# Performance work log

Hardware: AMD Instinct MI355X
Metric: run time of the kernel (lower is better)

## Reference

```python
import jax, jax.numpy as jnp
import numpy as np

B, T, R = 64, 256, 256          # batch, timepoints, n_rois (T==R required by bmm path)
H, NH, DH, FF, LAT, L = 256, 8, 32, 512, 64, 2
EPS = 1e-5


def layernorm(x, g, b):
    m = x.mean(-1, keepdims=True)
    v = ((x - m) ** 2).mean(-1, keepdims=True)
    return (x - m) / jnp.sqrt(v + EPS) * g + b


def leaky_relu(x):
    return jnp.where(x >= 0, x, 0.1 * x)


def setup_inputs() -> dict:
    key = jax.random.key(0)
    ks = iter(jax.random.split(key, 64))
    def nrm(shape, s=0.02):
        return jax.random.normal(next(ks), shape, jnp.float32) * s
    return {
        "x": jax.random.normal(next(ks), (B, T, R), jnp.float32),
        "node_view": jax.random.normal(next(ks), (B, R, R), jnp.float32) * 0.1,
        "edge_view": jax.random.normal(next(ks), (B, R, R), jnp.float32) * 0.1,
        "fp_w": nrm((H, R)), "fp_b": jnp.zeros((H,)),
        "fp_g": jnp.ones((H,)), "fp_beta": jnp.zeros((H,)),
        "qkv_w": nrm((L, 3 * H, H)), "qkv_b": jnp.zeros((L, 3 * H)),
        "attn_out_w": nrm((L, H, H)), "attn_out_b": jnp.zeros((L, H)),
        "ln1_g": jnp.ones((L, H)), "ln1_b": jnp.zeros((L, H)),
        "ff1_w": nrm((L, FF, H)), "ff1_b": jnp.zeros((L, FF)),
        "ff2_w": nrm((L, H, FF)), "ff2_b": jnp.zeros((L, H)),
        "ln2_g": jnp.ones((L, H)), "ln2_b": jnp.zeros((L, H)),
        "out_w": nrm((R, H)), "out_b": jnp.zeros((R,)),
        "mu_w1": nrm((H // 2, H)), "mu_b1": jnp.zeros((H // 2,)),
        "mu_g": jnp.ones((H // 2,)), "mu_beta": jnp.zeros((H // 2,)),
        "mu_w2": nrm((LAT, H // 2)), "mu_b2": jnp.zeros((LAT,)),
        "lv_w1": nrm((H // 2, H)), "lv_b1": jnp.zeros((H // 2,)),
        "lv_g": jnp.ones((H // 2,)), "lv_beta": jnp.zeros((H // 2,)),
        "lv_w2": nrm((LAT, H // 2)), "lv_b2": jnp.zeros((LAT,)),
    }


def reference(x, node_view, edge_view, fp_w, fp_b, fp_g, fp_beta,
              qkv_w, qkv_b, attn_out_w, attn_out_b, ln1_g, ln1_b,
              ff1_w, ff1_b, ff2_w, ff2_b, ln2_g, ln2_b,
              out_w, out_b, mu_w1, mu_b1, mu_g, mu_beta, mu_w2, mu_b2,
              lv_w1, lv_b1, lv_g, lv_beta, lv_w2, lv_b2):
    # graph-view message passing: bmm(x^T, view), averaged, transposed back
    xr = jnp.swapaxes(x, 1, 2)                           # [B,R,T]
    msg = 0.5 * (jnp.einsum('brt,btq->brq', xr, node_view)
                 + jnp.einsum('brt,btq->brq', xr, edge_view))
    h = jnp.swapaxes(msg, 1, 2)                          # [B,T,R]
    # feature_proj: Linear -> LayerNorm -> LeakyReLU(0.1) -> Dropout(eval)
    h = leaky_relu(layernorm(h @ fp_w.T + fp_b, fp_g, fp_beta))  # [B,T,H]
    # TransformerEncoder (post-norm, relu FFN, dropout=identity)
    scale = 1.0 / jnp.sqrt(jnp.float32(DH))
    for i in range(L):
        qkv = h @ qkv_w[i].T + qkv_b[i]                  # [B,T,3H]
        q, k, v = jnp.split(qkv, 3, axis=-1)
        q = q.reshape(B, T, NH, DH).transpose(0, 2, 1, 3)
        k = k.reshape(B, T, NH, DH).transpose(0, 2, 1, 3)
        v = v.reshape(B, T, NH, DH).transpose(0, 2, 1, 3)
        attn = jax.nn.softmax(jnp.einsum('bhqd,bhkd->bhqk', q, k) * scale, axis=-1)
        o = jnp.einsum('bhqk,bhkd->bhqd', attn, v).transpose(0, 2, 1, 3).reshape(B, T, H)
        o = o @ attn_out_w[i].T + attn_out_b[i]
        h = layernorm(h + o, ln1_g[i], ln1_b[i])
        f = jax.nn.relu(h @ ff1_w[i].T + ff1_b[i]) @ ff2_w[i].T + ff2_b[i]
        h = layernorm(h + f, ln2_g[i], ln2_b[i])
    # fresh linear (treated as fixed params) then batched Pearson correlation
    y = h @ out_w.T + out_b                              # [B,T,R]
    data = jnp.swapaxes(y, 1, 2)                         # [B,R,T]
    c = data - data.mean(-1, keepdims=True)
    std = jnp.sqrt((c ** 2).sum(-1, keepdims=True) / (T - 1))   # unbiased, like torch.std
    cn = c / (std + 1e-8)
    corr = jnp.einsum('brt,bst->brs', cn, cn) / (T - 1)
    corr = jnp.nan_to_num(jnp.clip(corr, -1.0, 1.0), nan=0.0)   # [B,R,R]
    # heads
    pooled = h.mean(axis=1)                              # [B,H]
    mu = leaky_relu(layernorm(pooled @ mu_w1.T + mu_b1, mu_g, mu_beta)) @ mu_w2.T + mu_b2
    logvar = leaky_relu(layernorm(pooled @ lv_w1.T + lv_b1, lv_g, lv_beta)) @ lv_w2.T + lv_b2
    return mu, logvar, corr
```

## Files before the change

### kernel.cpp

```cpp
#include <hip/hip_runtime.h>
#include <hip/hip_bf16.h>
#include <math.h>

#define BB 64
#define NLAYER 2

typedef __attribute__((ext_vector_type(8))) short bfrag;
typedef __attribute__((ext_vector_type(4))) float f4_t;

__device__ __forceinline__ float dot4(float4 a, float4 b, float acc) {
    acc = fmaf(a.x, b.x, acc);
    acc = fmaf(a.y, b.y, acc);
    acc = fmaf(a.z, b.z, acc);
    acc = fmaf(a.w, b.w, acc);
    return acc;
}

__device__ __forceinline__ ushort f2bf(float f) {
    uint32_t u = __float_as_uint(f);
    uint32_t r = (u + 0x7FFFu + ((u >> 16) & 1u)) >> 16;
    return (ushort)r;
}
__device__ __forceinline__ float bf2f(ushort u) {
    return __uint_as_float(((uint32_t)u) << 16);
}

__global__ __launch_bounds__(256) void k_cvt(
    const float* __restrict__ fp_w, const float* __restrict__ qkv_w,
    const float* __restrict__ aow, const float* __restrict__ f1w,
    const float* __restrict__ f2w, const float* __restrict__ outw,
    ushort* __restrict__ dst) {
    const int g = blockIdx.x;
    const size_t idx = (size_t)g * 2048 + threadIdx.x * 8;
    const float* src;
    size_t base;
    if (g < 32)       { src = fp_w;  base = 0; }
    else if (g < 224) { src = qkv_w; base = 65536; }
    else if (g < 288) { src = aow;   base = 458752; }
    else if (g < 416) { src = f1w;   base = 589824; }
    else if (g < 544) { src = f2w;   base = 851968; }
    else              { src = outw;  base = 1114112; }
    const float4* s4 = reinterpret_cast<const float4*>(src + (idx - base));
    float4 a = s4[0], b = s4[1];
    bfrag o;
    o[0] = (short)f2bf(a.x); o[1] = (short)f2bf(a.y);
    o[2] = (short)f2bf(a.z); o[3] = (short)f2bf(a.w);
    o[4] = (short)f2bf(b.x); o[5] = (short)f2bf(b.y);
    o[6] = (short)f2bf(b.z); o[7] = (short)f2bf(b.w);
    *reinterpret_cast<bfrag*>(dst + idx) = o;
}

template <int EPI, bool WF32, bool WBF>
__global__ __launch_bounds__(256) void k_mm(
    const ushort* __restrict__ A, const ushort* __restrict__ B,
    const float* __restrict__ bias, float* __restrict__ C,
    ushort* __restrict__ Cb, int K, int N,
    size_t aStr, size_t bStr, size_t cStr) {
    __shared__ __align__(16) ushort As[64 * 72];
    __shared__ __align__(16) ushort Bs[128 * 72];
    const int tid = threadIdx.x;
    const int m0 = blockIdx.x * 64, n0 = blockIdx.y * 128;
    const size_t z = blockIdx.z;
    const int w = tid >> 6, lane = tid & 63;
    const int wm = w >> 1, wn = w & 1;
    const int fr = lane & 15, fq = lane >> 4;

    const int arow = tid >> 2, akc = (tid & 3) * 16;
    const ushort* aS = A + z * aStr + (size_t)(m0 + arow) * K + akc;
    ushort* aD = &As[arow * 72 + akc];
    const int brow = tid >> 1, bkc = (tid & 1) * 32;
    const ushort* bS = B + z * bStr + (size_t)(n0 + brow) * K + bkc;
    ushort* bD = &Bs[brow * 72 + bkc];

    f4_t acc[2][4];
#pragma unroll
    for (int i = 0; i < 2; ++i)
#pragma unroll
        for (int j = 0; j < 4; ++j) acc[i][j] = (f4_t)0.f;

    bfrag ra0, ra1, rb0, rb1, rb2, rb3;
    {
        const bfrag* ap = reinterpret_cast<const bfrag*>(aS);
        ra0 = ap[0]; ra1 = ap[1];
        const bfrag* bp = reinterpret_cast<const bfrag*>(bS);
        rb0 = bp[0]; rb1 = bp[1]; rb2 = bp[2]; rb3 = bp[3];
    }

    for (int k0 = 0; k0 < K; k0 += 64) {
        reinterpret_cast<bfrag*>(aD)[0] = ra0;
        reinterpret_cast<bfrag*>(aD)[1] = ra1;
        reinterpret_cast<bfrag*>(bD)[0] = rb0;
        reinterpret_cast<bfrag*>(bD)[1] = rb1;
        reinterpret_cast<bfrag*>(bD)[2] = rb2;
        reinterpret_cast<bfrag*>(bD)[3] = rb3;
        __syncthreads();
        if (k0 + 64 < K) {
            const bfrag* ap = reinterpret_cast<const bfrag*>(aS + k0 + 64);
            ra0 = ap[0]; ra1 = ap[1];
            const bfrag* bp = reinterpret_cast<const bfrag*>(bS + k0 + 64);
            rb0 = bp[0]; rb1 = bp[1]; rb2 = bp[2]; rb3 = bp[3];
        }
#pragma unroll
        for (int ks = 0; ks < 2; ++ks) {
            const int kb = ks * 32 + fq * 8;
            bfrag af[2], bf[4];
#pragma unroll
            for (int fm = 0; fm < 2; ++fm)
                af[fm] = *reinterpret_cast<const bfrag*>(
                    &As[(wm * 32 + fm * 16 + fr) * 72 + kb]);
#pragma unroll
            for (int fn = 0; fn < 4; ++fn)
                bf[fn] = *reinterpret_cast<const bfrag*>(
                    &Bs[(wn * 64 + fn * 16 + fr) * 72 + kb]);
#pragma unroll
            for (int fm = 0; fm < 2; ++fm)
#pragma unroll
                for (int fn = 0; fn < 4; ++fn)
                    acc[fm][fn] = __builtin_amdgcn_mfma_f32_16x16x32_bf16(
                        bf[fn], af[fm], acc[fm][fn], 0, 0, 0);
        }
        __syncthreads();
    }

#pragma unroll
    for (int fn = 0; fn < 4; ++fn) {
        const int col0 = n0 + wn * 64 + fn * 16 + fq * 4;
        float4 bv = make_float4(0.f, 0.f, 0.f, 0.f);
        if (bias != nullptr)
            bv = *reinterpret_cast<const float4*>(&bias[col0]);
#pragma unroll
        for (int fm = 0; fm < 2; ++fm) {
            const int row = m0 + wm * 32 + fm * 16 + fr;
            float v0 = acc[fm][fn][0] + bv.x;
            float v1 = acc[fm][fn][1] + bv.y;
            float v2 = acc[fm][fn][2] + bv.z;
            float v3 = acc[fm][fn][3] + bv.w;
            if (EPI == 2) {
                v0 = fmaxf(v0, 0.f); v1 = fmaxf(v1, 0.f);
                v2 = fmaxf(v2, 0.f); v3 = fmaxf(v3, 0.f);
            }
            const size_t o = cStr * z + (size_t)row * N + col0;
            if (WF32) {
                float4 fv = {v0, v1, v2, v3};
                *reinterpret_cast<float4*>(&C[o]) = fv;
            }
            if (WBF) {
                ushort4 uv;
                uv.x = f2bf(v0); uv.y = f2bf(v1);
                uv.z = f2bf(v2); uv.w = f2bf(v3);
                *reinterpret_cast<ushort4*>(&Cb[o]) = uv;
            }
        }
    }
}

__global__ __launch_bounds__(256) void k_mmqkv(
    const ushort* __restrict__ A, const ushort* __restrict__ B,
    const float* __restrict__ bias, ushort* __restrict__ qb,
    ushort* __restrict__ kbuf, ushort* __restrict__ vtb) {
    __shared__ __align__(16) ushort As[64 * 72];
    __shared__ __align__(16) ushort Bs[128 * 72];
    const int tid = threadIdx.x;
    const int m0 = blockIdx.x * 64, n0 = blockIdx.y * 128;
    const int w = tid >> 6, lane = tid & 63;
    const int wm = w >> 1, wn = w & 1;
    const int fr = lane & 15, fq = lane >> 4;
    const int K = 256;

    const int arow = tid >> 2, akc = (tid & 3) * 16;
    const ushort* aS = A + (size_t)(m0 + arow) * K + akc;
    ushort* aD = &As[arow * 72 + akc];
    const int brow = tid >> 1, bkc = (tid & 1) * 32;
    const ushort* bS = B + (size_t)(n0 + brow) * K + bkc;
    ushort* bD = &Bs[brow * 72 + bkc];

    f4_t acc[2][4];
#pragma unroll
    for (int i = 0; i < 2; ++i)
#pragma unroll
        for (int j = 0; j < 4; ++j) acc[i][j] = (f4_t)0.f;

    bfrag ra0, ra1, rb0, rb1, rb2, rb3;
    {
        const bfrag* ap = reinterpret_cast<const bfrag*>(aS);
        ra0 = ap[0]; ra1 = ap[1];
        const bfrag* bp = reinterpret_cast<const bfrag*>(bS);
        rb0 = bp[0]; rb1 = bp[1]; rb2 = bp[2]; rb3 = bp[3];
    }

    for (int k0 = 0; k0 < K; k0 += 64) {
        reinterpret_cast<bfrag*>(aD)[0] = ra0;
        reinterpret_cast<bfrag*>(aD)[1] = ra1;
        reinterpret_cast<bfrag*>(bD)[0] = rb0;
        reinterpret_cast<bfrag*>(bD)[1] = rb1;
        reinterpret_cast<bfrag*>(bD)[2] = rb2;
        reinterpret_cast<bfrag*>(bD)[3] = rb3;
        __syncthreads();
        if (k0 + 64 < K) {
            const bfrag* ap = reinterpret_cast<const bfrag*>(aS + k0 + 64);
            ra0 = ap[0]; ra1 = ap[1];
            const bfrag* bp = reinterpret_cast<const bfrag*>(bS + k0 + 64);
            rb0 = bp[0]; rb1 = bp[1]; rb2 = bp[2]; rb3 = bp[3];
        }
#pragma unroll
        for (int ks = 0; ks < 2; ++ks) {
            const int kb = ks * 32 + fq * 8;
            bfrag af[2], bf[4];
#pragma unroll
            for (int fm = 0; fm < 2; ++fm)
                af[fm] = *reinterpret_cast<const bfrag*>(
                    &As[(wm * 32 + fm * 16 + fr) * 72 + kb]);
#pragma unroll
            for (int fn = 0; fn < 4; ++fn)
                bf[fn] = *reinterpret_cast<const bfrag*>(
                    &Bs[(wn * 64 + fn * 16 + fr) * 72 + kb]);
#pragma unroll
            for (int fm = 0; fm < 2; ++fm)
#pragma unroll
                for (int fn = 0; fn < 4; ++fn)
                    acc[fm][fn] = __builtin_amdgcn_mfma_f32_16x16x32_bf16(
                        bf[fn], af[fm], acc[fm][fn], 0, 0, 0);
        }
        __syncthreads();
    }

    const int sec = n0 >> 8;
#pragma unroll
    for (int fn = 0; fn < 4; ++fn) {
        const int col0 = n0 + wn * 64 + fn * 16 + fq * 4;
        const int hd = (col0 >> 5) & 7, dq = col0 & 31;
        const float4 bv = *reinterpret_cast<const float4*>(&bias[col0]);
#pragma unroll
        for (int fm = 0; fm < 2; ++fm) {
            const int row = m0 + wm * 32 + fm * 16 + fr;
            const int b = row >> 8, t = row & 255;
            const size_t bh = (size_t)b * 8 + hd;
            float v0 = acc[fm][fn][0] + bv.x;
            float v1 = acc[fm][fn][1] + bv.y;
            float v2 = acc[fm][fn][2] + bv.z;
            float v3 = acc[fm][fn][3] + bv.w;
            if (sec < 2) {
                ushort4 uv;
                uv.x = f2bf(v0); uv.y = f2bf(v1);
                uv.z = f2bf(v2); uv.w = f2bf(v3);
                ushort* dst = (sec == 0 ? qb : kbuf) + (bh * 256 + t) * 32 + dq;
                *reinterpret_cast<ushort4*>(dst) = uv;
            } else {
                ushort* dst = vtb + (bh * 32 + dq) * 256 + t;
                dst[0] = f2bf(v0);
                dst[256] = f2bf(v1);
                dst[512] = f2bf(v2);
                dst[768] = f2bf(v3);
            }
        }
    }
}

template <int ACT, bool RES>
__global__ __launch_bounds__(256) void k_mmln(
    const ushort* __restrict__ A, const ushort* __restrict__ W,
    const float* __restrict__ bias, const ushort* __restrict__ res,
    const float* __restrict__ g, const float* __restrict__ bt,
    ushort* __restrict__ outb, int K) {
    __shared__ __align__(16) ushort As[32 * 72];
    __shared__ __align__(16) ushort Bs[256 * 72];
    __shared__ float redS[32][4];
    __shared__ float redQ[32][4];
    const int tid = threadIdx.x;
    const int m0 = blockIdx.x * 32;
    const int w = tid >> 6, lane = tid & 63;
    const int fr = lane & 15, fq = lane >> 4;

    const int arow = tid >> 3, akc = (tid & 7) * 8;
    const ushort* aS = A + (size_t)(m0 + arow) * K + akc;
    ushort* aD = &As[arow * 72 + akc];
    const int brow = tid >> 1, bkc = (tid & 1) * 32;
    const ushort* bS0 = W + (size_t)brow * K + bkc;
    const ushort* bS1 = W + (size_t)(brow + 128) * K + bkc;
    ushort* bD0 = &Bs[brow * 72 + bkc];
    ushort* bD1 = &Bs[(brow + 128) * 72 + bkc];

    f4_t acc[2][4];
#pragma unroll
    for (int i = 0; i < 2; ++i)
#pragma unroll
        for (int j = 0; j < 4; ++j) acc[i][j] = (f4_t)0.f;

    bfrag ra, rb0, rb1, rb2, rb3, rc0, rc1, rc2, rc3;
    {
        ra = *reinterpret_cast<const bfrag*>(aS);
        const bfrag* bp0 = reinterpret_cast<const bfrag*>(bS0);
        rb0 = bp0[0]; rb1 = bp0[1]; rb2 = bp0[2]; rb3 = bp0[3];
        const bfrag* bp1 = reinterpret_cast<const bfrag*>(bS1);
        rc0 = bp1[0]; rc1 = bp1[1]; rc2 = bp1[2]; rc3 = bp1[3];
    }

    for (int k0 = 0; k0 < K; k0 += 64) {
        *reinterpret_cast<bfrag*>(aD) = ra;
        reinterpret_cast<bfrag*>(bD0)[0] = rb0;
        reinterpret_cast<bfrag*>(bD0)[1] = rb1;
        reinterpret_cast<bfrag*>(bD0)[2] = rb2;
        reinterpret_cast<bfrag*>(bD0)[3] = rb3;
        reinterpret_cast<bfrag*>(bD1)[0] = rc0;
        reinterpret_cast<bfrag*>(bD1)[1] = rc1;
        reinterpret_cast<bfrag*>(bD1)[2] = rc2;
        reinterpret_cast<bfrag*>(bD1)[3] = rc3;
        __syncthreads();
        if (k0 + 64 < K) {
            ra = *reinterpret_cast<const bfrag*>(aS + k0 + 64);
            const bfrag* bp0 = reinterpret_cast<const bfrag*>(bS0 + k0 + 64);
            rb0 = bp0[0]; rb1 = bp0[1]; rb2 = bp0[2]; rb3 = bp0[3];
            const bfrag* bp1 = reinterpret_cast<const bfrag*>(bS1 + k0 + 64);
            rc0 = bp1[0]; rc1 = bp1[1]; rc2 = bp1[2]; rc3 = bp1[3];
        }
#pragma unroll
        for (int ks = 0; ks < 2; ++ks) {
            const int kb = ks * 32 + fq * 8;
            bfrag af[2], bf[4];
#pragma unroll
            for (int fm = 0; fm < 2; ++fm)
                af[fm] = *reinterpret_cast<const bfrag*>(
                    &As[(fm * 16 + fr) * 72 + kb]);
#pragma unroll
            for (int fn = 0; fn < 4; ++fn)
                bf[fn] = *reinterpret_cast<const bfrag*>(
                    &Bs[(w * 64 + fn * 16 + fr) * 72 + kb]);
#pragma unroll
            for (int fm = 0; fm < 2; ++fm)
#pragma unroll
                for (int fn = 0; fn < 4; ++fn)
                    acc[fm][fn] = __builtin_amdgcn_mfma_f32_16x16x32_bf16(
                        bf[fn], af[fm], acc[fm][fn], 0, 0, 0);
        }
        __syncthreads();
    }

#pragma unroll
    for (int fn = 0; fn < 4; ++fn) {
        const int col0 = w * 64 + fn * 16 + fq * 4;
        const float4 bv = *reinterpret_cast<const float4*>(&bias[col0]);
#pragma unroll
        for (int fm = 0; fm < 2; ++fm) {
            const int row = fm * 16 + fr;
            float r0 = 0.f, r1 = 0.f, r2 = 0.f, r3 = 0.f;
            if (RES) {
                ushort4 r4 = *reinterpret_cast<const ushort4*>(
                    &res[(size_t)(m0 + row) * 256 + col0]);
                r0 = bf2f(r4.x); r1 = bf2f(r4.y);
                r2 = bf2f(r4.z); r3 = bf2f(r4.w);
            }
            acc[fm][fn][0] += bv.x + r0;
            acc[fm][fn][1] += bv.y + r1;
            acc[fm][fn][2] += bv.z + r2;
            acc[fm][fn][3] += bv.w + r3;
        }
    }
#pragma unroll
    for (int fm = 0; fm < 2; ++fm) {
        float s = 0.f, q = 0.f;
#pragma unroll
        for (int fn = 0; fn < 4; ++fn)
#pragma unroll
            for (int j = 0; j < 4; ++j) {
                const float v = acc[fm][fn][j];
                s += v;
                q += v * v;
            }
        s += __shfl_xor(s, 16); q += __shfl_xor(q, 16);
        s += __shfl_xor(s, 32); q += __shfl_xor(q, 32);
        if (fq == 0) {
            redS[fm * 16 + fr][w] = s;
            redQ[fm * 16 + fr][w] = q;
        }
    }
    __syncthreads();
#pragma unroll
    for (int fm = 0; fm < 2; ++fm) {
        const int row = fm * 16 + fr;
        const float S = redS[row][0] + redS[row][1] + redS[row][2] + redS[row][3];
        const float Q = redQ[row][0] + redQ[row][1] + redQ[row][2] + redQ[row][3];
        const float mean = S * (1.f / 256.f);
        const float var = Q * (1.f / 256.f) - mean * mean;
        const float rstd = rsqrtf(fmaxf(var, 0.f) + 1e-5f);
        const size_t rowoff = (size_t)(m0 + row) * 256;
#pragma unroll
        for (int fn = 0; fn < 4; ++fn) {
            const int col0 = w * 64 + fn * 16 + fq * 4;
            const float4 g4 = *reinterpret_cast<const float4*>(&g[col0]);
            const float4 b4 = *reinterpret_cast<const float4*>(&bt[col0]);
            float v0 = (acc[fm][fn][0] - mean) * rstd * g4.x + b4.x;
            float v1 = (acc[fm][fn][1] - mean) * rstd * g4.y + b4.y;
            float v2 = (acc[fm][fn][2] - mean) * rstd * g4.z + b4.z;
            float v3 = (acc[fm][fn][3] - mean) * rstd * g4.w + b4.w;
            if (ACT == 1) {
                v0 = v0 >= 0.f ? v0 : 0.1f * v0;
                v1 = v1 >= 0.f ? v1 : 0.1f * v1;
                v2 = v2 >= 0.f ? v2 : 0.1f * v2;
                v3 = v3 >= 0.f ? v3 : 0.1f * v3;
            }
            ushort4 uv;
            uv.x = f2bf(v0); uv.y = f2bf(v1);
            uv.z = f2bf(v2); uv.w = f2bf(v3);
            *reinterpret_cast<ushort4*>(&outb[rowoff + col0]) = uv;
        }
    }
}

__global__ __launch_bounds__(256) void k_attn3(
    const ushort* __restrict__ qb, const ushort* __restrict__ kbuf,
    const ushort* __restrict__ vtb, ushort* __restrict__ o) {
    __shared__ __align__(16) ushort Ps[4][64][40];
    const int hd = blockIdx.x, b = blockIdx.y;
    const size_t bh = (size_t)b * 8 + hd;
    const int tid = threadIdx.x;
    const int w = tid >> 6, lane = tid & 63;
    const int fr = lane & 15, fq = lane >> 4;

    const ushort* qB = qb + bh * 8192;
    const ushort* kB = kbuf + bh * 8192;
    const ushort* vB = vtb + bh * 8192;

    const int q0 = w * 64;
    bfrag qf[4];
#pragma unroll
    for (int fm = 0; fm < 4; ++fm)
        qf[fm] = *reinterpret_cast<const bfrag*>(
            qB + (size_t)(q0 + fm * 16 + fr) * 32 + fq * 8);

    f4_t oacc[4][2];
    float rs[4][4];
#pragma unroll
    for (int fm = 0; fm < 4; ++fm) {
        oacc[fm][0] = (f4_t)0.f;
        oacc[fm][1] = (f4_t)0.f;
#pragma unroll
        for (int j = 0; j < 4; ++j) rs[fm][j] = 0.f;
    }
    const f4_t zero4 = (f4_t)0.f;
    const float qsl = 0.17677669529663687f * 1.4426950408889634f;

    for (int kt = 0; kt < 8; ++kt) {
        bfrag kf0 = *reinterpret_cast<const bfrag*>(
            kB + (size_t)(kt * 32 + fr) * 32 + fq * 8);
        bfrag kf1 = *reinterpret_cast<const bfrag*>(
            kB + (size_t)(kt * 32 + 16 + fr) * 32 + fq * 8);
        f4_t s0[4], s1[4];
#pragma unroll
        for (int fm = 0; fm < 4; ++fm) {
            s0[fm] = __builtin_amdgcn_mfma_f32_16x16x32_bf16(qf[fm], kf0, zero4, 0, 0, 0);
            s1[fm] = __builtin_amdgcn_mfma_f32_16x16x32_bf16(qf[fm], kf1, zero4, 0, 0, 0);
        }
#pragma unroll
        for (int fm = 0; fm < 4; ++fm) {
#pragma unroll
            for (int j = 0; j < 4; ++j) {
                const int row = fm * 16 + fq * 4 + j;
                ushort u0 = f2bf(exp2f(s0[fm][j] * qsl));
                ushort u1 = f2bf(exp2f(s1[fm][j] * qsl));
                Ps[w][row][fr] = u0;
                Ps[w][row][16 + fr] = u1;
                rs[fm][j] += bf2f(u0) + bf2f(u1);
            }
        }
        bfrag vf0 = *reinterpret_cast<const bfrag*>(
            vB + (size_t)fr * 256 + kt * 32 + fq * 8);
        bfrag vf1 = *reinterpret_cast<const bfrag*>(
            vB + (size_t)(16 + fr) * 256 + kt * 32 + fq * 8);
        bfrag pf[4];
#pragma unroll
        for (int fm = 0; fm < 4; ++fm)
            pf[fm] = *reinterpret_cast<const bfrag*>(&Ps[w][fm * 16 + fr][fq * 8]);
#pragma unroll
        for (int fm = 0; fm < 4; ++fm) {
            oacc[fm][0] = __builtin_amdgcn_mfma_f32_16x16x32_bf16(pf[fm], vf0, oacc[fm][0], 0, 0, 0);
            oacc[fm][1] = __builtin_amdgcn_mfma_f32_16x16x32_bf16(pf[fm], vf1, oacc[fm][1], 0, 0, 0);
        }
    }

#pragma unroll
    for (int fm = 0; fm < 4; ++fm)
#pragma unroll
        for (int j = 0; j < 4; ++j) {
            float r = rs[fm][j];
            r += __shfl_xor(r, 1);
            r += __shfl_xor(r, 2);
            r += __shfl_xor(r, 4);
            r += __shfl_xor(r, 8);
            rs[fm][j] = 1.f / r;
        }
    ushort* ob = o + (size_t)b * 65536 + hd * 32;
#pragma unroll
    for (int fm = 0; fm < 4; ++fm) {
        const int qrow = q0 + fm * 16 + fq * 4;
#pragma unroll
        for (int j = 0; j < 4; ++j) {
            const float inv = rs[fm][j];
            ob[(size_t)(qrow + j) * 256 + fr] = f2bf(oacc[fm][0][j] * inv);
            ob[(size_t)(qrow + j) * 256 + 16 + fr] = f2bf(oacc[fm][1][j] * inv);
        }
    }
}

__global__ __launch_bounds__(256) void k_xpose_bmm(
    const float* __restrict__ x, const float* __restrict__ nv,
    const float* __restrict__ ev, ushort* __restrict__ At,
    ushort* __restrict__ Xt) {
    const int b = blockIdx.z;
    const int k0 = blockIdx.x * 64, i0 = blockIdx.y * 64;
    __shared__ float TA[64][65];
    __shared__ float TX[64][65];
    const size_t bb = (size_t)b * 65536;
    const int tid = threadIdx.x;
    const int lr = tid >> 4, lc = (tid & 15) * 4;
#pragma unroll
    for (int l = 0; l < 4; ++l) {
        const int row = lr + l * 16;
        const size_t gidx = bb + (size_t)(k0 + row) * 256 + i0 + lc;
        float4 n4 = *reinterpret_cast<const float4*>(nv + gidx);
        float4 e4 = *reinterpret_cast<const float4*>(ev + gidx);
        float4 x4 = *reinterpret_cast<const float4*>(x + gidx);
        TA[row][lc] = 0.5f * (n4.x + e4.x);
        TA[row][lc + 1] = 0.5f * (n4.y + e4.y);
        TA[row][lc + 2] = 0.5f * (n4.z + e4.z);
        TA[row][lc + 3] = 0.5f * (n4.w + e4.w);
        TX[row][lc] = x4.x;
        TX[row][lc + 1] = x4.y;
        TX[row][lc + 2] = x4.z;
        TX[row][lc + 3] = x4.w;
    }
    __syncthreads();
    const int i = tid & 63, kk = (tid >> 6) * 16;
    bfrag a0, a1, x0, x1;
#pragma unroll
    for (int e = 0; e < 8; ++e) {
        a0[e] = (short)f2bf(TA[kk + e][i]);
        a1[e] = (short)f2bf(TA[kk + 8 + e][i]);
        x0[e] = (short)f2bf(TX[kk + e][i]);
        x1[e] = (short)f2bf(TX[kk + 8 + e][i]);
    }
    const size_t o = bb + (size_t)(i0 + i) * 256 + k0 + kk;
    *reinterpret_cast<bfrag*>(At + o) = a0;
    *reinterpret_cast<bfrag*>(At + o + 8) = a1;
    *reinterpret_cast<bfrag*>(Xt + o) = x0;
    *reinterpret_cast<bfrag*>(Xt + o + 8) = x1;
}

__global__ __launch_bounds__(256) void k_rowstats(const ushort* __restrict__ yT,
                                                  float* __restrict__ stats) {
    const int b = blockIdx.y;
    const int r = blockIdx.x * 64 + (threadIdx.x >> 2);
    const int part = threadIdx.x & 3;
    const ushort* row = yT + (size_t)b * 65536 + (size_t)r * 256 + part * 64;
    float s = 0.f, q = 0.f;
#pragma unroll
    for (int i = 0; i < 8; ++i) {
        bfrag v = reinterpret_cast<const bfrag*>(row)[i];
#pragma unroll
        for (int e = 0; e < 8; ++e) {
            float f = bf2f((ushort)v[e]);
            s += f;
            q += f * f;
        }
    }
    s += __shfl_xor(s, 1); q += __shfl_xor(q, 1);
    s += __shfl_xor(s, 2); q += __shfl_xor(q, 2);
    if (part == 0) {
        const float mean = s * (1.f / 256.f);
        const float var = (q - s * mean) * (1.f / 255.f);
        const float stdv = sqrtf(fmaxf(var, 0.f));
        stats[b * 512 + r] = mean;
        stats[b * 512 + 256 + r] = 1.f / (stdv + 1e-8f);
    }
}

__global__ __launch_bounds__(256) void k_corr2(
    const ushort* __restrict__ A, const float* __restrict__ stats,
    float* __restrict__ C) {
    __shared__ __align__(16) ushort As[64 * 72];
    __shared__ __align__(16) ushort Bs[128 * 72];
    const int tid = threadIdx.x;
    const int m0 = blockIdx.x * 64, n0 = blockIdx.y * 128;
    const size_t z = blockIdx.z;
    const int w = tid >> 6, lane = tid & 63;
    const int wm = w >> 1, wn = w & 1;
    const int fr = lane & 15, fq = lane >> 4;
    const int K = 256;

    const int arow = tid >> 2, akc = (tid & 3) * 16;
    const ushort* aS = A + z * 65536 + (size_t)(m0 + arow) * K + akc;
    ushort* aD = &As[arow * 72 + akc];
    const int brow = tid >> 1, bkc = (tid & 1) * 32;
    const ushort* bS = A + z * 65536 + (size_t)(n0 + brow) * K + bkc;
    ushort* bD = &Bs[brow * 72 + bkc];

    f4_t acc[2][4];
#pragma unroll
    for (int i = 0; i < 2; ++i)
#pragma unroll
        for (int j = 0; j < 4; ++j) acc[i][j] = (f4_t)0.f;

    bfrag ra0, ra1, rb0, rb1, rb2, rb3;
    {
        const bfrag* ap = reinterpret_cast<const bfrag*>(aS);
        ra0 = ap[0]; ra1 = ap[1];
        const bfrag* bp = reinterpret_cast<const bfrag*>(bS);
        rb0 = bp[0]; rb1 = bp[1]; rb2 = bp[2]; rb3 = bp[3];
    }

    for (int k0 = 0; k0 < K; k0 += 64) {
        reinterpret_cast<bfrag*>(aD)[0] = ra0;
        reinterpret_cast<bfrag*>(aD)[1] = ra1;
        reinterpret_cast<bfrag*>(bD)[0] = rb0;
        reinterpret_cast<bfrag*>(bD)[1] = rb1;
        reinterpret_cast<bfrag*>(bD)[2] = rb2;
        reinterpret_cast<bfrag*>(bD)[3] = rb3;
        __syncthreads();
        if (k0 + 64 < K) {
            const bfrag* ap = reinterpret_cast<const bfrag*>(aS + k0 + 64);
            ra0 = ap[0]; ra1 = ap[1];
            const bfrag* bp = reinterpret_cast<const bfrag*>(bS + k0 + 64);
            rb0 = bp[0]; rb1 = bp[1]; rb2 = bp[2]; rb3 = bp[3];
        }
#pragma unroll
        for (int ks = 0; ks < 2; ++ks) {
            const int kb = ks * 32 + fq * 8;
            bfrag af[2], bf[4];
#pragma unroll
            for (int fm = 0; fm < 2; ++fm)
                af[fm] = *reinterpret_cast<const bfrag*>(
                    &As[(wm * 32 + fm * 16 + fr) * 72 + kb]);
#pragma unroll
            for (int fn = 0; fn < 4; ++fn)
                bf[fn] = *reinterpret_cast<const bfrag*>(
                    &Bs[(wn * 64 + fn * 16 + fr) * 72 + kb]);
#pragma unroll
            for (int fm = 0; fm < 2; ++fm)
#pragma unroll
                for (int fn = 0; fn < 4; ++fn)
                    acc[fm][fn] = __builtin_amdgcn_mfma_f32_16x16x32_bf16(
                        bf[fn], af[fm], acc[fm][fn], 0, 0, 0);
        }
        __syncthreads();
    }

    const float* st = stats + z * 512;
#pragma unroll
    for (int fn = 0; fn < 4; ++fn) {
        const int col0 = n0 + wn * 64 + fn * 16 + fq * 4;
        const float4 muj = *reinterpret_cast<const float4*>(&st[col0]);
        const float4 isj = *reinterpret_cast<const float4*>(&st[256 + col0]);
#pragma unroll
        for (int fm = 0; fm < 2; ++fm) {
            const int row = m0 + wm * 32 + fm * 16 + fr;
            const float mui = st[row];
            const float isi = st[256 + row] * (1.f / 255.f);
            float v0 = (acc[fm][fn][0] - 256.f * mui * muj.x) * isi * isj.x;
            float v1 = (acc[fm][fn][1] - 256.f * mui * muj.y) * isi * isj.y;
            float v2 = (acc[fm][fn][2] - 256.f * mui * muj.z) * isi * isj.z;
            float v3 = (acc[fm][fn][3] - 256.f * mui * muj.w) * isi * isj.w;
            if (v0 != v0) v0 = 0.f;
            if (v1 != v1) v1 = 0.f;
            if (v2 != v2) v2 = 0.f;
            if (v3 != v3) v3 = 0.f;
            v0 = fminf(1.f, fmaxf(-1.f, v0));
            v1 = fminf(1.f, fmaxf(-1.f, v1));
            v2 = fminf(1.f, fmaxf(-1.f, v2));
            v3 = fminf(1.f, fmaxf(-1.f, v3));
            float4 fv = {v0, v1, v2, v3};
            *reinterpret_cast<float4*>(
                &C[z * 65536 + (size_t)row * 256 + col0]) = fv;
        }
    }
}

__global__ __launch_bounds__(512) void k_poolhead(
    const ushort* __restrict__ h,
    const float* __restrict__ mw1, const float* __restrict__ mb1,
    const float* __restrict__ mg, const float* __restrict__ mbt,
    const float* __restrict__ mw2, const float* __restrict__ mb2,
    const float* __restrict__ lw1, const float* __restrict__ lb1,
    const float* __restrict__ lg, const float* __restrict__ lbt,
    const float* __restrict__ lw2, const float* __restrict__ lb2,
    float* __restrict__ outp) {
    const int b = blockIdx.x, tid = threadIdx.x;
    __shared__ float pp[2][256];
    __shared__ float pooled[256];
    __shared__ float rS[4], rQ[4];
    __shared__ float t1[2][128];

    {
        const int c = tid & 255, tc = tid >> 8;
        const ushort* hb = h + (size_t)b * 65536 + (size_t)tc * 128 * 256 + c;
        float s = 0.f;
        for (int t = 0; t < 128; ++t) s += bf2f(hb[(size_t)t * 256]);
        pp[tc][c] = s;
    }
    __syncthreads();
    if (tid < 256) pooled[tid] = (pp[0][tid] + pp[1][tid]) * (1.f / 256.f);
    __syncthreads();

    float a = 0.f;
    if (tid < 256) {
        const int hd = tid >> 7, u = tid & 127;
        const float* w1 = hd ? lw1 : mw1;
        const float* b1 = hd ? lb1 : mb1;
        a = b1[u];
        const float4* w1v = reinterpret_cast<const float4*>(w1 + (size_t)u * 256);
#pragma unroll 4
        for (int k4 = 0; k4 < 64; ++k4) {
            float4 wv = w1v[k4];
            float4 p = *reinterpret_cast<const float4*>(&pooled[k4 * 4]);
            a = dot4(p, wv, a);
        }
        float s = a, q = a * a;
#pragma unroll
        for (int m = 1; m < 64; m <<= 1) {
            s += __shfl_xor(s, m);
            q += __shfl_xor(q, m);
        }
        if ((tid & 63) == 0) { rS[tid >> 6] = s; rQ[tid >> 6] = q; }
    }
    __syncthreads();
    if (tid < 256) {
        const int hd = tid >> 7, u = tid & 127;
        const float* g = hd ? lg : mg;
        const float* bt = hd ? lbt : mbt;
        const float S = rS[hd * 2] + rS[hd * 2 + 1];
        const float Q = rQ[hd * 2] + rQ[hd * 2 + 1];
        const float mean = S * (1.f / 128.f);
        const float var = Q * (1.f / 128.f) - mean * mean;
        const float rstd = rsqrtf(fmaxf(var, 0.f) + 1e-5f);
        float v = (a - mean) * rstd * g[u] + bt[u];
        v = v >= 0.f ? v : 0.1f * v;
        t1[hd][u] = v;
    }
    __syncthreads();
    if (tid < 128) {
        const int hd = tid >> 6, ou = tid & 63;
        const float* w2 = hd ? lw2 : mw2;
        const float* b2 = hd ? lb2 : mb2;
        float o = b2[ou];
        const float* w2r = w2 + (size_t)ou * 128;
#pragma unroll 4
        for (int c = 0; c < 128; ++c) o = fmaf(t1[hd][c], w2r[c], o);
        outp[hd * 4096 + b * 64 + ou] = o;
    }
}

extern "C" void kernel_launch(void* const* d_in, const int* in_sizes, int n_in,
                              void* d_out, int out_size, void* d_ws, size_t ws_size,
                              hipStream_t stream) {
    const float* x = (const float*)d_in[0];
    const float* nv = (const float*)d_in[1];
    const float* ev = (const float*)d_in[2];
    const float* fp_w = (const float*)d_in[3];
    const float* fp_b = (const float*)d_in[4];
    const float* fp_g = (const float*)d_in[5];
    const float* fp_beta = (const float*)d_in[6];
    const float* qkv_w = (const float*)d_in[7];
    const float* qkv_b = (const float*)d_in[8];
    const float* aow = (const float*)d_in[9];
    const float* aob = (const float*)d_in[10];
    const float* ln1g = (const float*)d_in[11];
    const float* ln1b = (const float*)d_in[12];
    const float* f1w = (const float*)d_in[13];
    const float* f1b = (const float*)d_in[14];
    const float* f2w = (const float*)d_in[15];
    const float* f2b = (const float*)d_in[16];
    const float* ln2g = (const float*)d_in[17];
    const float* ln2b = (const float*)d_in[18];
    const float* outw = (const float*)d_in[19];
    const float* outb = (const float*)d_in[20];
    const float* muw1 = (const float*)d_in[21];
    const float* mub1 = (const float*)d_in[22];
    const float* mug = (const float*)d_in[23];
    const float* mubt = (const float*)d_in[24];
    const float* muw2 = (const float*)d_in[25];
    const float* mub2 = (const float*)d_in[26];
    const float* lvw1 = (const float*)d_in[27];
    const float* lvb1 = (const float*)d_in[28];
    const float* lvg = (const float*)d_in[29];
    const float* lvbt = (const float*)d_in[30];
    const float* lvw2 = (const float*)d_in[31];
    const float* lvb2 = (const float*)d_in[32];

    float* out = (float*)d_out;
    float* ws = (float*)d_ws;

    float* stats = ws;
    ushort* ub = (ushort*)(ws + 32768);
    ushort* wh_bf = ub;
    ushort* At = ub + 4194304;
    ushort* Xt = ub + 8388608;
    ushort* o_bf = ub + 16777216;
    ushort* h0_bf = o_bf;
    ushort* f1_bf = ub + 20971520;
    ushort* qb = ub + 29360128;
    ushort* kb = ub + 33554432;
    ushort* vtb = ub + 37748736;
    ushort* yT = ub + 41943040;
    ushort* wbf = ub + 46137344;

    k_cvt<<<576, 256, 0, stream>>>(fp_w, qkv_w, aow, f1w, f2w, outw, wbf);

    k_xpose_bmm<<<dim3(4, 4, BB), 256, 0, stream>>>(x, nv, ev, At, Xt);
    k_mm<0, false, true><<<dim3(4, 2, BB), 256, 0, stream>>>(
        At, Xt, nullptr, nullptr, h0_bf, 256, 256, 65536, 65536, 65536);

    k_mmln<1, false><<<512, 256, 0, stream>>>(
        h0_bf, wbf, fp_b, nullptr, fp_g, fp_beta, wh_bf, 256);

    for (int l = 0; l < NLAYER; ++l) {
        k_mmqkv<<<dim3(256, 6), 256, 0, stream>>>(
            wh_bf, wbf + 65536 + (size_t)l * 196608, qkv_b + l * 768,
            qb, kb, vtb);
        k_attn3<<<dim3(8, BB), 256, 0, stream>>>(qb, kb, vtb, o_bf);
        k_mmln<0, true><<<512, 256, 0, stream>>>(
            o_bf, wbf + 458752 + (size_t)l * 65536, aob + l * 256,
            wh_bf, ln1g + l * 256, ln1b + l * 256, wh_bf, 256);
        k_mm<2, false, true><<<dim3(256, 4, 1), 256, 0, stream>>>(
            wh_bf, wbf + 589824 + (size_t)l * 131072, f1b + l * 512,
            nullptr, f1_bf, 256, 512, 0, 0, 0);
        k_mmln<0, true><<<512, 256, 0, stream>>>(
            f1_bf, wbf + 851968 + (size_t)l * 131072, f2b + l * 256,
            wh_bf, ln2g + l * 256, ln2b + l * 256, wh_bf, 512);
    }

    k_mm<0, false, true><<<dim3(4, 2, BB), 256, 0, stream>>>(
        wbf + 1114112, wh_bf, nullptr, nullptr, yT, 256, 256, 0, 65536, 65536);

    k_rowstats<<<dim3(4, BB), 256, 0, stream>>>(yT, stats);
    k_corr2<<<dim3(4, 2, BB), 256, 0, stream>>>(yT, stats, out + 8192);

    k_poolhead<<<BB, 512, 0, stream>>>(
        wh_bf, muw1, mub1, mug, mubt, muw2, mub2,
        lvw1, lvb1, lvg, lvbt, lvw2, lvb2, out);
}
```

Baseline: 239.1 us.

## Use direct global-to-LDS loads and 128x128 tiles in GEMM kernels

Replaces the register-staged, padded-LDS GEMM loads with `__builtin_amdgcn_global_load_lds` direct copies into an unpadded 64-wide LDS layout. The output tile grows from 64x128 to 128x128, so each wave computes 4x4 MFMA fragments. This applies to the generic matmul, the QKV projection and the correlation kernel, with grids halved to match. It aims to cut VGPR staging and raise arithmetic intensity per block. In exchange it drops the register prefetch of the next K slice, halves the number of blocks, and the unpadded layout may cause LDS bank conflicts on fragment reads.

```diff
diff --git a/kernel.cpp b/kernel.cpp
--- a/kernel.cpp
+++ b/kernel.cpp
@@ -23,6 +23,12 @@
 }
 __device__ __forceinline__ float bf2f(ushort u) {
     return __uint_as_float(((uint32_t)u) << 16);
+}
+
+__device__ __forceinline__ void gll16(const ushort* g, ushort* l) {
+    __builtin_amdgcn_global_load_lds(
+        (const __attribute__((address_space(1))) void*)g,
+        (__attribute__((address_space(3))) void*)l, 16, 0, 0);
 }
 
 __global__ __launch_bounds__(256) void k_cvt(
@@ -50,75 +56,66 @@
     *reinterpret_cast<bfrag*>(dst + idx) = o;
 }
 
+#define MM97_STAGE(SRC, LDS, KSTRIDE)                                        \
+    {                                                                        \
+        _Pragma("unroll")                                                    \
+        for (int c = 0; c < 4; ++c) {                                        \
+            const int rr = (w << 5) + (c << 3) + (lane >> 3);                \
+            gll16(SRC + (size_t)rr * (KSTRIDE) + k0 + ((lane & 7) << 3),     \
+                  LDS + (((w << 5) + (c << 3)) << 6));                       \
+        }                                                                    \
+    }
+
+#define MM97_COMPUTE()                                                       \
+    _Pragma("unroll")                                                        \
+    for (int ks = 0; ks < 2; ++ks) {                                         \
+        const int kb = ks * 32 + fq * 8;                                     \
+        bfrag af[4], bfv[4];                                                 \
+        _Pragma("unroll")                                                    \
+        for (int fm = 0; fm < 4; ++fm)                                       \
+            af[fm] = *reinterpret_cast<const bfrag*>(                        \
+                &As[((wm * 64 + fm * 16 + fr) << 6) + kb]);                  \
+        _Pragma("unroll")                                                    \
+        for (int fn = 0; fn < 4; ++fn)                                       \
+            bfv[fn] = *reinterpret_cast<const bfrag*>(                       \
+                &Bs[((wn * 64 + fn * 16 + fr) << 6) + kb]);                  \
+        _Pragma("unroll")                                                    \
+        for (int fm = 0; fm < 4; ++fm)                                       \
+            _Pragma("unroll")                                                \
+            for (int fn = 0; fn < 4; ++fn)                                   \
+                acc[fm][fn] = __builtin_amdgcn_mfma_f32_16x16x32_bf16(       \
+                    bfv[fn], af[fm], acc[fm][fn], 0, 0, 0);                  \
+    }
+
 template <int EPI, bool WF32, bool WBF>
-__global__ __launch_bounds__(256) void k_mm(
+__global__ __launch_bounds__(256) void k_mm97(
     const ushort* __restrict__ A, const ushort* __restrict__ B,
     const float* __restrict__ bias, float* __restrict__ C,
     ushort* __restrict__ Cb, int K, int N,
     size_t aStr, size_t bStr, size_t cStr) {
-    __shared__ __align__(16) ushort As[64 * 72];
-    __shared__ __align__(16) ushort Bs[128 * 72];
+    __shared__ __align__(16) ushort As[128 * 64];
+    __shared__ __align__(16) ushort Bs[128 * 64];
     const int tid = threadIdx.x;
-    const int m0 = blockIdx.x * 64, n0 = blockIdx.y * 128;
+    const int m0 = blockIdx.x * 128, n0 = blockIdx.y * 128;
     const size_t z = blockIdx.z;
     const int w = tid >> 6, lane = tid & 63;
     const int wm = w >> 1, wn = w & 1;
     const int fr = lane & 15, fq = lane >> 4;
 
-    const int arow = tid >> 2, akc = (tid & 3) * 16;
-    const ushort* aS = A + z * aStr + (size_t)(m0 + arow) * K + akc;
-    ushort* aD = &As[arow * 72 + akc];
-    const int brow = tid >> 1, bkc = (tid & 1) * 32;
-    const ushort* bS = B + z * bStr + (size_t)(n0 + brow) * K + bkc;
-    ushort* bD = &Bs[brow * 72 + bkc];
-
-    f4_t acc[2][4];
-#pragma unroll
-    for (int i = 0; i < 2; ++i)
+    const ushort* aB = A + z * aStr + (size_t)m0 * K;
+    const ushort* bB = B + z * bStr + (size_t)n0 * K;
+
+    f4_t acc[4][4];
+#pragma unroll
+    for (int i = 0; i < 4; ++i)
 #pragma unroll
         for (int j = 0; j < 4; ++j) acc[i][j] = (f4_t)0.f;
 
-    bfrag ra0, ra1, rb0, rb1, rb2, rb3;
-    {
-        const bfrag* ap = reinterpret_cast<const bfrag*>(aS);
-        ra0 = ap[0]; ra1 = ap[1];
-        const bfrag* bp = reinterpret_cast<const bfrag*>(bS);
-        rb0 = bp[0]; rb1 = bp[1]; rb2 = bp[2]; rb3 = bp[3];
-    }
-
     for (int k0 = 0; k0 < K; k0 += 64) {
-        reinterpret_cast<bfrag*>(aD)[0] = ra0;
-        reinterpret_cast<bfrag*>(aD)[1] = ra1;
-        reinterpret_cast<bfrag*>(bD)[0] = rb0;
-        reinterpret_cast<bfrag*>(bD)[1] = rb1;
-        reinterpret_cast<bfrag*>(bD)[2] = rb2;
-        reinterpret_cast<bfrag*>(bD)[3] = rb3;
+        MM97_STAGE(aB, As, K)
+        MM97_STAGE(bB, Bs, K)
         __syncthreads();
-        if (k0 + 64 < K) {
-            const bfrag* ap = reinterpret_cast<const bfrag*>(aS + k0 + 64);
-            ra0 = ap[0]; ra1 = ap[1];
-            const bfrag* bp = reinterpret_cast<const bfrag*>(bS + k0 + 64);
-            rb0 = bp[0]; rb1 = bp[1]; rb2 = bp[2]; rb3 = bp[3];
-        }
-#pragma unroll
-        for (int ks = 0; ks < 2; ++ks) {
-            const int kb = ks * 32 + fq * 8;
-            bfrag af[2], bf[4];
-#pragma unroll
-            for (int fm = 0; fm < 2; ++fm)
-                af[fm] = *reinterpret_cast<const bfrag*>(
-                    &As[(wm * 32 + fm * 16 + fr) * 72 + kb]);
-#pragma unroll
-            for (int fn = 0; fn < 4; ++fn)
-                bf[fn] = *reinterpret_cast<const bfrag*>(
-                    &Bs[(wn * 64 + fn * 16 + fr) * 72 + kb]);
-#pragma unroll
-            for (int fm = 0; fm < 2; ++fm)
-#pragma unroll
-                for (int fn = 0; fn < 4; ++fn)
-                    acc[fm][fn] = __builtin_amdgcn_mfma_f32_16x16x32_bf16(
-                        bf[fn], af[fm], acc[fm][fn], 0, 0, 0);
-        }
+        MM97_COMPUTE()
         __syncthreads();
     }
 
@@ -129,8 +126,8 @@
         if (bias != nullptr)
             bv = *reinterpret_cast<const float4*>(&bias[col0]);
 #pragma unroll
-        for (int fm = 0; fm < 2; ++fm) {
-            const int row = m0 + wm * 32 + fm * 16 + fr;
+        for (int fm = 0; fm < 4; ++fm) {
+            const int row = m0 + wm * 64 + fm * 16 + fr;
             float v0 = acc[fm][fn][0] + bv.x;
             float v1 = acc[fm][fn][1] + bv.y;
             float v2 = acc[fm][fn][2] + bv.z;
@@ -154,73 +151,33 @@
     }
 }
 
-__global__ __launch_bounds__(256) void k_mmqkv(
+__global__ __launch_bounds__(256) void k_mmqkv97(
     const ushort* __restrict__ A, const ushort* __restrict__ B,
     const float* __restrict__ bias, ushort* __restrict__ qb,
     ushort* __restrict__ kbuf, ushort* __restrict__ vtb) {
-    __shared__ __align__(16) ushort As[64 * 72];
-    __shared__ __align__(16) ushort Bs[128 * 72];
+    __shared__ __align__(16) ushort As[128 * 64];
+    __shared__ __align__(16) ushort Bs[128 * 64];
     const int tid = threadIdx.x;
-    const int m0 = blockIdx.x * 64, n0 = blockIdx.y * 128;
+    const int m0 = blockIdx.x * 128, n0 = blockIdx.y * 128;
     const int w = tid >> 6, lane = tid & 63;
     const int wm = w >> 1, wn = w & 1;
     const int fr = lane & 15, fq = lane >> 4;
     const int K = 256;
 
-    const int arow = tid >> 2, akc = (tid & 3) * 16;
-    const ushort* aS = A + (size_t)(m0 + arow) * K + akc;
-    ushort* aD = &As[arow * 72 + akc];
-    const int brow = tid >> 1, bkc = (tid & 1) * 32;
-    const ushort* bS = B + (size_t)(n0 + brow) * K + bkc;
-    ushort* bD = &Bs[brow * 72 + bkc];
-
-    f4_t acc[2][4];
-#pragma unroll
-    for (int i = 0; i < 2; ++i)
+    const ushort* aB = A + (size_t)m0 * K;
+    const ushort* bB = B + (size_t)n0 * K;
+
+    f4_t acc[4][4];
+#pragma unroll
+    for (int i = 0; i < 4; ++i)
 #pragma unroll
         for (int j = 0; j < 4; ++j) acc[i][j] = (f4_t)0.f;
 
-    bfrag ra0, ra1, rb0, rb1, rb2, rb3;
-    {
-        const bfrag* ap = reinterpret_cast<const bfrag*>(aS);
-        ra0 = ap[0]; ra1 = ap[1];
-        const bfrag* bp = reinterpret_cast<const bfrag*>(bS);
-        rb0 = bp[0]; rb1 = bp[1]; rb2 = bp[2]; rb3 = bp[3];
-    }
-
     for (int k0 = 0; k0 < K; k0 += 64) {
-        reinterpret_cast<bfrag*>(aD)[0] = ra0;
-        reinterpret_cast<bfrag*>(aD)[1] = ra1;
-        reinterpret_cast<bfrag*>(bD)[0] = rb0;
-        reinterpret_cast<bfrag*>(bD)[1] = rb1;
-        reinterpret_cast<bfrag*>(bD)[2] = rb2;
-        reinterpret_cast<bfrag*>(bD)[3] = rb3;
+        MM97_STAGE(aB, As, K)
+        MM97_STAGE(bB, Bs, K)
         __syncthreads();
-        if (k0 + 64 < K) {
-            const bfrag* ap = reinterpret_cast<const bfrag*>(aS + k0 + 64);
-            ra0 = ap[0]; ra1 = ap[1];
-            const bfrag* bp = reinterpret_cast<const bfrag*>(bS + k0 + 64);
-            rb0 = bp[0]; rb1 = bp[1]; rb2 = bp[2]; rb3 = bp[3];
-        }
-#pragma unroll
-        for (int ks = 0; ks < 2; ++ks) {
-            const int kb = ks * 32 + fq * 8;
-            bfrag af[2], bf[4];
-#pragma unroll
-            for (int fm = 0; fm < 2; ++fm)
-                af[fm] = *reinterpret_cast<const bfrag*>(
-                    &As[(wm * 32 + fm * 16 + fr) * 72 + kb]);
-#pragma unroll
-            for (int fn = 0; fn < 4; ++fn)
-                bf[fn] = *reinterpret_cast<const bfrag*>(
-                    &Bs[(wn * 64 + fn * 16 + fr) * 72 + kb]);
-#pragma unroll
-            for (int fm = 0; fm < 2; ++fm)
-#pragma unroll
-                for (int fn = 0; fn < 4; ++fn)
-                    acc[fm][fn] = __builtin_amdgcn_mfma_f32_16x16x32_bf16(
-                        bf[fn], af[fm], acc[fm][fn], 0, 0, 0);
-        }
+        MM97_COMPUTE()
         __syncthreads();
     }
 
@@ -231,8 +188,8 @@
         const int hd = (col0 >> 5) & 7, dq = col0 & 31;
         const float4 bv = *reinterpret_cast<const float4*>(&bias[col0]);
 #pragma unroll
-        for (int fm = 0; fm < 2; ++fm) {
-            const int row = m0 + wm * 32 + fm * 16 + fr;
+        for (int fm = 0; fm < 4; ++fm) {
+            const int row = m0 + wm * 64 + fm * 16 + fr;
             const int b = row >> 8, t = row & 255;
             const size_t bh = (size_t)b * 8 + hd;
             float v0 = acc[fm][fn][0] + bv.x;
@@ -256,6 +213,66 @@
     }
 }
 
+__global__ __launch_bounds__(256) void k_corr97(
+    const ushort* __restrict__ A, const float* __restrict__ stats,
+    float* __restrict__ C) {
+    __shared__ __align__(16) ushort As[128 * 64];
+    __shared__ __align__(16) ushort Bs[128 * 64];
+    const int tid = threadIdx.x;
+    const int m0 = blockIdx.x * 128, n0 = blockIdx.y * 128;
+    const size_t z = blockIdx.z;
+    const int w = tid >> 6, lane = tid & 63;
+    const int wm = w >> 1, wn = w & 1;
+    const int fr = lane & 15, fq = lane >> 4;
+    const int K = 256;
+
+    const ushort* aB = A + z * 65536 + (size_t)m0 * K;
+    const ushort* bB = A + z * 65536 + (size_t)n0 * K;
+
+    f4_t acc[4][4];
+#pragma unroll
+    for (int i = 0; i < 4; ++i)
+#pragma unroll
+        for (int j = 0; j < 4; ++j) acc[i][j] = (f4_t)0.f;
+
+    for (int k0 = 0; k0 < K; k0 += 64) {
+        MM97_STAGE(aB, As, K)
+        MM97_STAGE(bB, Bs, K)
+        __syncthreads();
+        MM97_COMPUTE()
+        __syncthreads();
+    }
+
+    const float* st = stats + z * 512;
+#pragma unroll
+    for (int fn = 0; fn < 4; ++fn) {
+        const int col0 = n0 + wn * 64 + fn * 16 + fq * 4;
+        const float4 muj = *reinterpret_cast<const float4*>(&st[col0]);
+        const float4 isj = *reinterpret_cast<const float4*>(&st[256 + col0]);
+#pragma unroll
+        for (int fm = 0; fm < 4; ++fm) {
+            const int row = m0 + wm * 64 + fm * 16 + fr;
+            const float mui = st[row];
+            const float isi = st[256 + row] * (1.f / 255.f);
+            float v0 = (acc[fm][fn][0] - 256.f * mui * muj.x) * isi * isj.x;
+            float v1 = (acc[fm][fn][1] - 256.f * mui * muj.y) * isi * isj.y;
+            float v2 = (acc[fm][fn][2] - 256.f * mui * muj.z) * isi * isj.z;
+            float v3 = (acc[fm][fn][3] - 256.f * mui * muj.w) * isi * isj.w;
+            if (v0 != v0) v0 = 0.f;
+            if (v1 != v1) v1 = 0.f;
+            if (v2 != v2) v2 = 0.f;
+            if (v3 != v3) v3 = 0.f;
+            v0 = fminf(1.f, fmaxf(-1.f, v0));
+            v1 = fminf(1.f, fmaxf(-1.f, v1));
+            v2 = fminf(1.f, fmaxf(-1.f, v2));
+            v3 = fminf(1.f, fmaxf(-1.f, v3));
+            float4 fv = {v0, v1, v2, v3};
+            *reinterpret_cast<float4*>(
+                &C[z * 65536 + (size_t)row * 256 + col0]) = fv;
+        }
+    }
+}
+
 template <int ACT, bool RES>
 __global__ __launch_bounds__(256) void k_mmln(
     const ushort* __restrict__ A, const ushort* __restrict__ W,
@@ -570,106 +587,6 @@
         const float stdv = sqrtf(fmaxf(var, 0.f));
         stats[b * 512 + r] = mean;
         stats[b * 512 + 256 + r] = 1.f / (stdv + 1e-8f);
-    }
-}
-
-__global__ __launch_bounds__(256) void k_corr2(
-    const ushort* __restrict__ A, const float* __restrict__ stats,
-    float* __restrict__ C) {
-    __shared__ __align__(16) ushort As[64 * 72];
-    __shared__ __align__(16) ushort Bs[128 * 72];
-    const int tid = threadIdx.x;
-    const int m0 = blockIdx.x * 64, n0 = blockIdx.y * 128;
-    const size_t z = blockIdx.z;
-    const int w = tid >> 6, lane = tid & 63;
-    const int wm = w >> 1, wn = w & 1;
-    const int fr = lane & 15, fq = lane >> 4;
-    const int K = 256;
-
-    const int arow = tid >> 2, akc = (tid & 3) * 16;
-    const ushort* aS = A + z * 65536 + (size_t)(m0 + arow) * K + akc;
-    ushort* aD = &As[arow * 72 + akc];
-    const int brow = tid >> 1, bkc = (tid & 1) * 32;
-    const ushort* bS = A + z * 65536 + (size_t)(n0 + brow) * K + bkc;
-    ushort* bD = &Bs[brow * 72 + bkc];
-
-    f4_t acc[2][4];
-#pragma unroll
-    for (int i = 0; i < 2; ++i)
-#pragma unroll
-        for (int j = 0; j < 4; ++j) acc[i][j] = (f4_t)0.f;
-
-    bfrag ra0, ra1, rb0, rb1, rb2, rb3;
-    {
-        const bfrag* ap = reinterpret_cast<const bfrag*>(aS);
-        ra0 = ap[0]; ra1 = ap[1];
-        const bfrag* bp = reinterpret_cast<const bfrag*>(bS);
-        rb0 = bp[0]; rb1 = bp[1]; rb2 = bp[2]; rb3 = bp[3];
-    }
-
-    for (int k0 = 0; k0 < K; k0 += 64) {
-        reinterpret_cast<bfrag*>(aD)[0] = ra0;
-        reinterpret_cast<bfrag*>(aD)[1] = ra1;
-        reinterpret_cast<bfrag*>(bD)[0] = rb0;
-        reinterpret_cast<bfrag*>(bD)[1] = rb1;
-        reinterpret_cast<bfrag*>(bD)[2] = rb2;
-        reinterpret_cast<bfrag*>(bD)[3] = rb3;
-        __syncthreads();
-        if (k0 + 64 < K) {
-            const bfrag* ap = reinterpret_cast<const bfrag*>(aS + k0 + 64);
-            ra0 = ap[0]; ra1 = ap[1];
-            const bfrag* bp = reinterpret_cast<const bfrag*>(bS + k0 + 64);
-            rb0 = bp[0]; rb1 = bp[1]; rb2 = bp[2]; rb3 = bp[3];
-        }
-#pragma unroll
-        for (int ks = 0; ks < 2; ++ks) {
-            const int kb = ks * 32 + fq * 8;
-            bfrag af[2], bf[4];
-#pragma unroll
-            for (int fm = 0; fm < 2; ++fm)
-                af[fm] = *reinterpret_cast<const bfrag*>(
-                    &As[(wm * 32 + fm * 16 + fr) * 72 + kb]);
-#pragma unroll
-            for (int fn = 0; fn < 4; ++fn)
-                bf[fn] = *reinterpret_cast<const bfrag*>(
-                    &Bs[(wn * 64 + fn * 16 + fr) * 72 + kb]);
-#pragma unroll
-            for (int fm = 0; fm < 2; ++fm)
-#pragma unroll
-                for (int fn = 0; fn < 4; ++fn)
-                    acc[fm][fn] = __builtin_amdgcn_mfma_f32_16x16x32_bf16(
-                        bf[fn], af[fm], acc[fm][fn], 0, 0, 0);
-        }
-        __syncthreads();
-    }
-
-    const float* st = stats + z * 512;
-#pragma unroll
-    for (int fn = 0; fn < 4; ++fn) {
-        const int col0 = n0 + wn * 64 + fn * 16 + fq * 4;
-        const float4 muj = *reinterpret_cast<const float4*>(&st[col0]);
-        const float4 isj = *reinterpret_cast<const float4*>(&st[256 + col0]);
-#pragma unroll
-        for (int fm = 0; fm < 2; ++fm) {
-            const int row = m0 + wm * 32 + fm * 16 + fr;
-            const float mui = st[row];
-            const float isi = st[256 + row] * (1.f / 255.f);
-            float v0 = (acc[fm][fn][0] - 256.f * mui * muj.x) * isi * isj.x;
-            float v1 = (acc[fm][fn][1] - 256.f * mui * muj.y) * isi * isj.y;
-            float v2 = (acc[fm][fn][2] - 256.f * mui * muj.z) * isi * isj.z;
-            float v3 = (acc[fm][fn][3] - 256.f * mui * muj.w) * isi * isj.w;
-            if (v0 != v0) v0 = 0.f;
-            if (v1 != v1) v1 = 0.f;
-            if (v2 != v2) v2 = 0.f;
-            if (v3 != v3) v3 = 0.f;
-            v0 = fminf(1.f, fmaxf(-1.f, v0));
-            v1 = fminf(1.f, fmaxf(-1.f, v1));
-            v2 = fminf(1.f, fmaxf(-1.f, v2));
-            v3 = fminf(1.f, fmaxf(-1.f, v3));
-            float4 fv = {v0, v1, v2, v3};
-            *reinterpret_cast<float4*>(
-                &C[z * 65536 + (size_t)row * 256 + col0]) = fv;
-        }
     }
 }
 
@@ -804,21 +721,21 @@
     k_cvt<<<576, 256, 0, stream>>>(fp_w, qkv_w, aow, f1w, f2w, outw, wbf);
 
     k_xpose_bmm<<<dim3(4, 4, BB), 256, 0, stream>>>(x, nv, ev, At, Xt);
-    k_mm<0, false, true><<<dim3(4, 2, BB), 256, 0, stream>>>(
+    k_mm97<0, false, true><<<dim3(2, 2, BB), 256, 0, stream>>>(
         At, Xt, nullptr, nullptr, h0_bf, 256, 256, 65536, 65536, 65536);
 
     k_mmln<1, false><<<512, 256, 0, stream>>>(
         h0_bf, wbf, fp_b, nullptr, fp_g, fp_beta, wh_bf, 256);
 
     for (int l = 0; l < NLAYER; ++l) {
-        k_mmqkv<<<dim3(256, 6), 256, 0, stream>>>(
+        k_mmqkv97<<<dim3(128, 6), 256, 0, stream>>>(
             wh_bf, wbf + 65536 + (size_t)l * 196608, qkv_b + l * 768,
             qb, kb, vtb);
         k_attn3<<<dim3(8, BB), 256, 0, stream>>>(qb, kb, vtb, o_bf);
         k_mmln<0, true><<<512, 256, 0, stream>>>(
             o_bf, wbf + 458752 + (size_t)l * 65536, aob + l * 256,
             wh_bf, ln1g + l * 256, ln1b + l * 256, wh_bf, 256);
-        k_mm<2, false, true><<<dim3(256, 4, 1), 256, 0, stream>>>(
+        k_mm97<2, false, true><<<dim3(128, 4, 1), 256, 0, stream>>>(
             wh_bf, wbf + 589824 + (size_t)l * 131072, f1b + l * 512,
             nullptr, f1_bf, 256, 512, 0, 0, 0);
         k_mmln<0, true><<<512, 256, 0, stream>>>(
@@ -826,11 +743,11 @@
             wh_bf, ln2g + l * 256, ln2b + l * 256, wh_bf, 512);
     }
 
-    k_mm<0, false, true><<<dim3(4, 2, BB), 256, 0, stream>>>(
+    k_mm97<0, false, true><<<dim3(2, 2, BB), 256, 0, stream>>>(
         wbf + 1114112, wh_bf, nullptr, nullptr, yT, 256, 256, 0, 65536, 65536);
 
     k_rowstats<<<dim3(4, BB), 256, 0, stream>>>(yT, stats);
-    k_corr2<<<dim3(4, 2, BB), 256, 0, stream>>>(yT, stats, out + 8192);
+    k_corr97<<<dim3(2, 2, BB), 256, 0, stream>>>(yT, stats, out + 8192);
 
     k_poolhead<<<BB, 512, 0, stream>>>(
         wh_bf, muw1, mub1, mug, mubt, muw2, mub2,
```

After: 236.3 us. No clear change (-1.2%).
